# Optimization experiments

Measured on AMD Instinct MI355X. Metric: run time of the kernel, lower is better.

The kernel has to match this reference:

```python
import jax, jax.numpy as jnp
import numpy as np
import math

D = 512
CAT_VOCAB = 512
TIME_START, TIME_STEPS = 512, 1000
NOTE_START, NOTE_RANGE = 1512, 128
VEL_START, VEL_BINS = 1640, 32
DUR_START, DUR_STEPS = 1672, 1000
VOCAB = 2672


def setup_inputs() -> dict:
    key = jax.random.key(0)
    ks = jax.random.split(key, 16)
    tokens = jax.random.randint(ks[0], (8, 8192), 0, VOCAB)
    token_emb = jax.random.normal(ks[1], (CAT_VOCAB, D), jnp.float32) * 0.02
    token_emb = token_emb.at[0].set(0.0)  # padding_idx=0 row is zero
    return {
        'tokens': tokens,
        'token_emb': token_emb,
        'time_lin_w': jax.random.normal(ks[2], (D // 2,), jnp.float32),
        'time_lin_b': jax.random.normal(ks[3], (D // 2,), jnp.float32),
        'time_w': jax.random.normal(ks[4], (D // 2,), jnp.float32),
        'time_b': jax.random.normal(ks[5], (D // 2,), jnp.float32),
        'vel_w1': jax.random.normal(ks[6], (D // 2,), jnp.float32),
        'vel_b1': jax.random.normal(ks[7], (D // 2,), jnp.float32),
        'vel_w2': jax.random.normal(ks[8], (D, D // 2), jnp.float32) * 0.05,
        'vel_b2': jax.random.normal(ks[9], (D,), jnp.float32),
        'vel_ln_g': jnp.ones((D,), jnp.float32),
        'vel_ln_b': jnp.zeros((D,), jnp.float32),
        'dur_lin_w': jax.random.normal(ks[10], (D // 2,), jnp.float32),
        'dur_lin_b': jax.random.normal(ks[11], (D // 2,), jnp.float32),
        'dur_w': jax.random.normal(ks[12], (D // 2,), jnp.float32),
        'dur_b': jax.random.normal(ks[13], (D // 2,), jnp.float32),
    }


def _time2vec(t, max_steps, lin_w, lin_b, w, b):
    tn = t.astype(jnp.float32)[..., None] / max_steps        # [B,S,1]
    linear = tn * lin_w + lin_b                              # [B,S,D/2]
    periodic = jnp.sin(tn * w + b)                           # [B,S,D/2]
    return jnp.concatenate([linear, periodic], axis=-1)


def _pitch_embed(p):
    pf = p.astype(jnp.float32)
    octave = jnp.floor(pf / 12.0)
    semitone = jnp.mod(pf, 12.0)
    i = jnp.arange(D // 4, dtype=jnp.float32)                # [D/4]
    div = 2.0 ** i
    ph_oct = octave[..., None] / div                         # [B,S,D/4]
    ph_sem = semitone[..., None] * (math.pi / 6.0) * (i + 1.0)
    # interleave (sin oct, cos oct, sin sem, cos sem) per group of 4
    emb = jnp.stack([jnp.sin(ph_oct), jnp.cos(ph_oct),
                     jnp.sin(ph_sem), jnp.cos(ph_sem)], axis=-1)
    return emb.reshape(*p.shape, D)


def _vel_embed(v, w1, b1, w2, b2, g, beta):
    vn = v.astype(jnp.float32)[..., None] / VEL_BINS         # [B,S,1]
    h = jax.nn.gelu(vn * w1 + b1, approximate=False)         # [B,S,D/2]
    e = jnp.einsum('bsh,dh->bsd', h, w2) + b2                # [B,S,D]
    mu = e.mean(-1, keepdims=True)
    var = ((e - mu) ** 2).mean(-1, keepdims=True)
    return g * (e - mu) / jnp.sqrt(var + 1e-5) + beta


def reference(tokens, token_emb, time_lin_w, time_lin_b, time_w, time_b,
              vel_w1, vel_b1, vel_w2, vel_b2, vel_ln_g, vel_ln_b,
              dur_lin_w, dur_lin_b, dur_w, dur_b):
    cat_mask = tokens < CAT_VOCAB
    time_mask = (tokens >= TIME_START) & (tokens < TIME_START + TIME_STEPS)
    note_mask = (tokens >= NOTE_START) & (tokens < NOTE_START + NOTE_RANGE)
    vel_mask = (tokens >= VEL_START) & (tokens < VEL_START + VEL_BINS)
    dur_mask = (tokens >= DUR_START) & (tokens < DUR_START + DUR_STEPS)

    safe_idx = jnp.clip(tokens, 0, CAT_VOCAB - 1)
    out = jnp.where(cat_mask[..., None], token_emb[safe_idx], 0.0)

    t_emb = _time2vec(tokens - TIME_START, float(TIME_STEPS),
                      time_lin_w, time_lin_b, time_w, time_b)
    p_emb = _pitch_embed(tokens - NOTE_START)
    v_emb = _vel_embed(tokens - VEL_START, vel_w1, vel_b1, vel_w2, vel_b2,
                       vel_ln_g, vel_ln_b)
    d_emb = _time2vec(tokens - DUR_START, float(DUR_STEPS),
                      dur_lin_w, dur_lin_b, dur_w, dur_b)

    out = jnp.where(time_mask[..., None], t_emb, out)
    out = jnp.where(note_mask[..., None], p_emb, out)
    out = jnp.where(vel_mask[..., None], v_emb, out)
    out = jnp.where(dur_mask[..., None], d_emb, out)
    return out
```

## Files before the change

kernel.cpp:

```cpp
#include <hip/hip_runtime.h>
#include <math.h>

#define DD 512
#define CAT_VOCAB 512
#define TIME_START 512
#define TIME_STEPS 1000
#define NOTE_START 1512
#define NOTE_RANGE 128
#define VEL_START 1640
#define VEL_BINS 32
#define DUR_START 1672
#define DUR_STEPS 1000
#define VOCAB 2672

typedef float f32x4 __attribute__((ext_vector_type(4)));

__device__ __forceinline__ float gelu_exact(float x) {
    return 0.5f * x * (1.0f + erff(x * 0.70710678118654752440f));
}

__device__ __forceinline__ float fsin(float x) {
    float r = x * 0.15915494309189535f;
    r = r - floorf(r);
    return __builtin_amdgcn_sinf(r);
}
__device__ __forceinline__ float fcos(float x) {
    float r = x * 0.15915494309189535f;
    r = r - floorf(r);
    return __builtin_amdgcn_cosf(r);
}

__global__ __launch_bounds__(256) void vel_e_kernel(
    const float* __restrict__ vel_w1, const float* __restrict__ vel_b1,
    const float* __restrict__ vel_w2, const float* __restrict__ vel_b2,
    float* __restrict__ e_tab,
    float* __restrict__ stats)
{
    __shared__ float e_lds[64];

    const int blk = blockIdx.x;
    const int b   = blk >> 3;
    const int o   = blk & 7;
    const float vn = (float)b / 32.0f;
    const int tid = threadIdx.x;
    const int lane = tid & 63;
    const int wave = tid >> 6;

    const float4 w1v = *(const float4*)(vel_w1 + lane * 4);
    const float4 b1v = *(const float4*)(vel_b1 + lane * 4);
    float4 hv;
    hv.x = gelu_exact(vn * w1v.x + b1v.x);
    hv.y = gelu_exact(vn * w1v.y + b1v.y);
    hv.z = gelu_exact(vn * w1v.z + b1v.z);
    hv.w = gelu_exact(vn * w1v.w + b1v.w);

    const int rbase = o * 64 + wave * 16;
    for (int rg = 0; rg < 16; rg += 8) {
        float p[8];
        #pragma unroll
        for (int k = 0; k < 8; ++k) {
            const int d = rbase + rg + k;
            const float4 w2v = *(const float4*)(vel_w2 + (size_t)d * 256 + lane * 4);
            p[k] = w2v.x * hv.x + w2v.y * hv.y + w2v.z * hv.z + w2v.w * hv.w;
        }
        #pragma unroll
        for (int off = 32; off > 0; off >>= 1) {
            #pragma unroll
            for (int k = 0; k < 8; ++k) p[k] += __shfl_xor(p[k], off);
        }
        #pragma unroll
        for (int k = 0; k < 8; ++k) {
            if (lane == k) e_lds[wave * 16 + rg + k] = p[k] + vel_b2[rbase + rg + k];
        }
    }
    __syncthreads();

    if (tid < 64) {
        const float e = e_lds[tid];
        e_tab[(size_t)b * DD + o * 64 + tid] = e;
        float s = e, q = e * e;
        #pragma unroll
        for (int off = 32; off > 0; off >>= 1) {
            s += __shfl_xor(s, off);
            q += __shfl_xor(q, off);
        }
        if (tid == 0) {
            stats[((size_t)b * 8 + o) * 2]     = s;
            stats[((size_t)b * 8 + o) * 2 + 1] = q;
        }
    }
}

__global__ __launch_bounds__(256) void direct_kernel(
    const int* __restrict__ tokens,
    const float* __restrict__ token_emb,
    const float* __restrict__ time_lin_w, const float* __restrict__ time_lin_b,
    const float* __restrict__ time_w,     const float* __restrict__ time_b,
    const float* __restrict__ dur_lin_w,  const float* __restrict__ dur_lin_b,
    const float* __restrict__ dur_w,      const float* __restrict__ dur_b,
    const float* __restrict__ vel_ln_g,   const float* __restrict__ vel_ln_b,
    const float* __restrict__ e_tab,      const float* __restrict__ stats,
    float* __restrict__ out, int total_chunks)
{
    const int c = blockIdx.x * 256 + threadIdx.x;
    if (c >= total_chunks) return;

    const int tok = c >> 7;
    const int ch  = c & 127;
    const int d   = ch * 4;
    const int t   = tokens[tok];

    f32x4 v;

    if (t < CAT_VOCAB) {
        v = *(const f32x4*)(token_emb + (size_t)t * DD + d);
    } else if (t < NOTE_START || t >= DUR_START) {
        const bool is_time = (t < NOTE_START);
        const int start = is_time ? TIME_START : DUR_START;
        const float tn = (float)(t - start) / 1000.0f;
        if (ch < 64) {
            const float* lw = is_time ? time_lin_w : dur_lin_w;
            const float* lb = is_time ? time_lin_b : dur_lin_b;
            const float4 w = *(const float4*)(lw + d);
            const float4 b = *(const float4*)(lb + d);
            v.x = tn * w.x + b.x; v.y = tn * w.y + b.y;
            v.z = tn * w.z + b.z; v.w = tn * w.w + b.w;
        } else {
            const float* pw = is_time ? time_w : dur_w;
            const float* pb = is_time ? time_b : dur_b;
            const float4 w = *(const float4*)(pw + d - 256);
            const float4 b = *(const float4*)(pb + d - 256);
            v.x = fsin(tn * w.x + b.x); v.y = fsin(tn * w.y + b.y);
            v.z = fsin(tn * w.z + b.z); v.w = fsin(tn * w.w + b.w);
        }
    } else if (t < VEL_START) {
        const int p = t - NOTE_START;
        const float oct = (float)(p / 12);
        const float sem = (float)(p % 12);
        const float po = oct * __builtin_amdgcn_exp2f(-(float)ch);
        const float ps = sem * 0.52359877559829887308f * ((float)ch + 1.0f);
        v.x = fsin(po); v.y = fcos(po); v.z = fsin(ps); v.w = fcos(ps);
    } else {
        const int bin = t - VEL_START;
        const f32x4 e = *(const f32x4*)(e_tab + (size_t)bin * DD + d);
        float s = 0.0f, q = 0.0f;
        #pragma unroll
        for (int o = 0; o < 8; ++o) {
            s += stats[((size_t)bin * 8 + o) * 2];
            q += stats[((size_t)bin * 8 + o) * 2 + 1];
        }
        const float mu  = s * (1.0f / 512.0f);
        const float var = q * (1.0f / 512.0f) - mu * mu;
        const float inv = 1.0f / sqrtf(var + 1e-5f);
        const float4 g  = *(const float4*)(vel_ln_g + d);
        const float4 be = *(const float4*)(vel_ln_b + d);
        v.x = g.x * (e.x - mu) * inv + be.x;
        v.y = g.y * (e.y - mu) * inv + be.y;
        v.z = g.z * (e.z - mu) * inv + be.z;
        v.w = g.w * (e.w - mu) * inv + be.w;
    }

    __builtin_nontemporal_store(v, (f32x4*)(out + (size_t)c * 4));
}

__global__ __launch_bounds__(256) void music_emb_fallback(
    const int* __restrict__ tokens,
    const float* __restrict__ token_emb,
    const float* __restrict__ time_lin_w, const float* __restrict__ time_lin_b,
    const float* __restrict__ time_w,     const float* __restrict__ time_b,
    const float* __restrict__ vel_w1,     const float* __restrict__ vel_b1,
    const float* __restrict__ vel_w2,     const float* __restrict__ vel_b2,
    const float* __restrict__ vel_ln_g,   const float* __restrict__ vel_ln_b,
    const float* __restrict__ dur_lin_w,  const float* __restrict__ dur_lin_b,
    const float* __restrict__ dur_w,      const float* __restrict__ dur_b,
    float* __restrict__ out, int n_tokens)
{
    const int wave = threadIdx.x >> 6;
    const int lane = threadIdx.x & 63;
    const int tok_idx = blockIdx.x * 4 + wave;
    if (tok_idx >= n_tokens) return;

    const int t = tokens[tok_idx];
    float* __restrict__ orow = out + (size_t)tok_idx * DD;
    const int d0 = lane * 4;
    const int d1 = 256 + lane * 4;
    float4 r0, r1;

    if (t < CAT_VOCAB) {
        r0 = *(const float4*)(token_emb + (size_t)t * DD + d0);
        r1 = *(const float4*)(token_emb + (size_t)t * DD + d1);
    } else if (t < NOTE_START || (t >= DUR_START && t < DUR_START + DUR_STEPS)) {
        const bool is_time = (t < NOTE_START);
        const float* lw = is_time ? time_lin_w : dur_lin_w;
        const float* lb = is_time ? time_lin_b : dur_lin_b;
        const float* pw = is_time ? time_w    : dur_w;
        const float* pb = is_time ? time_b    : dur_b;
        const int start = is_time ? TIME_START : DUR_START;
        const float tn = (float)(t - start) / 1000.0f;
        float a[4], p[4];
        #pragma unroll
        for (int k = 0; k < 4; ++k) {
            a[k] = tn * lw[d0 + k] + lb[d0 + k];
            p[k] = sinf(tn * pw[d0 + k] + pb[d0 + k]);
        }
        r0 = make_float4(a[0], a[1], a[2], a[3]);
        r1 = make_float4(p[0], p[1], p[2], p[3]);
    } else if (t < NOTE_START + NOTE_RANGE) {
        const int p = t - NOTE_START;
        const float oct = (float)(p / 12);
        const float sem = (float)(p % 12);
        const float cc = 0.52359877559829887308f;
        {
            const float i = (float)lane;
            const float po = oct * exp2f(-i);
            const float ps = (sem * cc) * (i + 1.0f);
            r0 = make_float4(sinf(po), cosf(po), sinf(ps), cosf(ps));
        }
        {
            const float i = (float)(64 + lane);
            const float po = oct * exp2f(-i);
            const float ps = (sem * cc) * (i + 1.0f);
            r1 = make_float4(sinf(po), cosf(po), sinf(ps), cosf(ps));
        }
    } else if (t < VEL_START + VEL_BINS) {
        const float vn = (float)(t - VEL_START) / 32.0f;
        float hj[4];
        #pragma unroll
        for (int k = 0; k < 4; ++k) {
            const float x = vn * vel_w1[d0 + k] + vel_b1[d0 + k];
            hj[k] = gelu_exact(x);
        }
        float e0[4], e1[4];
        #pragma unroll
        for (int k = 0; k < 4; ++k) { e0[k] = vel_b2[d0 + k]; e1[k] = vel_b2[d1 + k]; }
        for (int src = 0; src < 64; ++src) {
            const float h0 = __shfl(hj[0], src);
            const float h1 = __shfl(hj[1], src);
            const float h2 = __shfl(hj[2], src);
            const float h3 = __shfl(hj[3], src);
            const int j = src << 2;
            #pragma unroll
            for (int k = 0; k < 4; ++k) {
                const float4 wa = *(const float4*)(vel_w2 + (size_t)(d0 + k) * 256 + j);
                const float4 wb = *(const float4*)(vel_w2 + (size_t)(d1 + k) * 256 + j);
                e0[k] += h0 * wa.x + h1 * wa.y + h2 * wa.z + h3 * wa.w;
                e1[k] += h0 * wb.x + h1 * wb.y + h2 * wb.z + h3 * wb.w;
            }
        }
        float s1 = 0.0f;
        #pragma unroll
        for (int k = 0; k < 4; ++k) s1 += e0[k] + e1[k];
        #pragma unroll
        for (int off = 32; off > 0; off >>= 1) s1 += __shfl_xor(s1, off);
        const float mu = s1 * (1.0f / 512.0f);
        float s2 = 0.0f;
        #pragma unroll
        for (int k = 0; k < 4; ++k) {
            const float a = e0[k] - mu, bb = e1[k] - mu;
            s2 += a * a + bb * bb;
        }
        #pragma unroll
        for (int off = 32; off > 0; off >>= 1) s2 += __shfl_xor(s2, off);
        const float inv = 1.0f / sqrtf(s2 * (1.0f / 512.0f) + 1e-5f);
        #pragma unroll
        for (int k = 0; k < 4; ++k) {
            e0[k] = vel_ln_g[d0 + k] * (e0[k] - mu) * inv + vel_ln_b[d0 + k];
            e1[k] = vel_ln_g[d1 + k] * (e1[k] - mu) * inv + vel_ln_b[d1 + k];
        }
        r0 = make_float4(e0[0], e0[1], e0[2], e0[3]);
        r1 = make_float4(e1[0], e1[1], e1[2], e1[3]);
    } else {
        r0 = make_float4(0.f, 0.f, 0.f, 0.f);
        r1 = make_float4(0.f, 0.f, 0.f, 0.f);
    }

    *(float4*)(orow + d0) = r0;
    *(float4*)(orow + d1) = r1;
}

extern "C" void kernel_launch(void* const* d_in, const int* in_sizes, int n_in,
                              void* d_out, int out_size, void* d_ws, size_t ws_size,
                              hipStream_t stream) {
    const int*   tokens     = (const int*)  d_in[0];
    const float* token_emb  = (const float*)d_in[1];
    const float* time_lin_w = (const float*)d_in[2];
    const float* time_lin_b = (const float*)d_in[3];
    const float* time_w     = (const float*)d_in[4];
    const float* time_b     = (const float*)d_in[5];
    const float* vel_w1     = (const float*)d_in[6];
    const float* vel_b1     = (const float*)d_in[7];
    const float* vel_w2     = (const float*)d_in[8];
    const float* vel_b2     = (const float*)d_in[9];
    const float* vel_ln_g   = (const float*)d_in[10];
    const float* vel_ln_b   = (const float*)d_in[11];
    const float* dur_lin_w  = (const float*)d_in[12];
    const float* dur_lin_b  = (const float*)d_in[13];
    const float* dur_w      = (const float*)d_in[14];
    const float* dur_b      = (const float*)d_in[15];
    float* out = (float*)d_out;

    const int n_tokens = in_sizes[0];
    const size_t e_bytes     = (size_t)VEL_BINS * DD * sizeof(float);
    const size_t stats_bytes = (size_t)VEL_BINS * 8 * 2 * sizeof(float);

    if (ws_size >= e_bytes + stats_bytes) {
        float* e_tab = (float*)d_ws;
        float* stats = (float*)((char*)d_ws + e_bytes);

        hipLaunchKernelGGL(vel_e_kernel, dim3(VEL_BINS * 8), dim3(256), 0, stream,
                           vel_w1, vel_b1, vel_w2, vel_b2, e_tab, stats);

        const int total_chunks = n_tokens * (DD / 4);
        const int blocks = (total_chunks + 255) / 256;
        hipLaunchKernelGGL(direct_kernel, dim3(blocks), dim3(256), 0, stream,
                           tokens, token_emb,
                           time_lin_w, time_lin_b, time_w, time_b,
                           dur_lin_w, dur_lin_b, dur_w, dur_b,
                           vel_ln_g, vel_ln_b, e_tab, stats,
                           out, total_chunks);
    } else {
        const int blocks = (n_tokens + 3) / 4;
        hipLaunchKernelGGL(music_emb_fallback, dim3(blocks), dim3(256), 0, stream,
                           tokens, token_emb,
                           time_lin_w, time_lin_b, time_w, time_b,
                           vel_w1, vel_b1, vel_w2, vel_b2, vel_ln_g, vel_ln_b,
                           dur_lin_w, dur_lin_b, dur_w, dur_b,
                           out, n_tokens);
    }
}
```

Before: 31.12 us.

## Map one wave per token in direct kernel and split velocity table work finer

The main kernel now gives each token to a single wavefront, with each lane writing two float4 chunks. Before, each thread handled one 4-float chunk. This removes per-chunk branch divergence within a wave, reads the token id once per wave, and merges the linear and periodic halves into one thread. The velocity precompute kernel is split into 16 slices per bin instead of 8, giving twice as many blocks each doing one pass of 8 rows. The fallback kernel switches to fast sin/cos/exp2 intrinsics, and the fast path now requires the token count to be a multiple of 4.

Result: slower. 32.79 us (+5.4%).

```diff
diff --git a/kernel.cpp b/kernel.cpp
--- a/kernel.cpp
+++ b/kernel.cpp
@@ -36,11 +36,11 @@
     float* __restrict__ e_tab,
     float* __restrict__ stats)
 {
-    __shared__ float e_lds[64];
+    __shared__ float e_lds[32];
 
     const int blk = blockIdx.x;
-    const int b   = blk >> 3;
-    const int o   = blk & 7;
+    const int b   = blk >> 4;
+    const int sx  = blk & 15;
     const float vn = (float)b / 32.0f;
     const int tid = threadIdx.x;
     const int lane = tid & 63;
@@ -54,39 +54,36 @@
     hv.z = gelu_exact(vn * w1v.z + b1v.z);
     hv.w = gelu_exact(vn * w1v.w + b1v.w);
 
-    const int rbase = o * 64 + wave * 16;
-    for (int rg = 0; rg < 16; rg += 8) {
-        float p[8];
-        #pragma unroll
-        for (int k = 0; k < 8; ++k) {
-            const int d = rbase + rg + k;
-            const float4 w2v = *(const float4*)(vel_w2 + (size_t)d * 256 + lane * 4);
-            p[k] = w2v.x * hv.x + w2v.y * hv.y + w2v.z * hv.z + w2v.w * hv.w;
-        }
-        #pragma unroll
-        for (int off = 32; off > 0; off >>= 1) {
-            #pragma unroll
-            for (int k = 0; k < 8; ++k) p[k] += __shfl_xor(p[k], off);
-        }
-        #pragma unroll
-        for (int k = 0; k < 8; ++k) {
-            if (lane == k) e_lds[wave * 16 + rg + k] = p[k] + vel_b2[rbase + rg + k];
-        }
+    const int rbase = sx * 32 + wave * 8;
+    float p[8];
+    #pragma unroll
+    for (int k = 0; k < 8; ++k) {
+        const float4 w2v = *(const float4*)(vel_w2 + (size_t)(rbase + k) * 256 + lane * 4);
+        p[k] = w2v.x * hv.x + w2v.y * hv.y + w2v.z * hv.z + w2v.w * hv.w;
+    }
+    #pragma unroll
+    for (int off = 32; off > 0; off >>= 1) {
+        #pragma unroll
+        for (int k = 0; k < 8; ++k) p[k] += __shfl_xor(p[k], off);
+    }
+    #pragma unroll
+    for (int k = 0; k < 8; ++k) {
+        if (lane == k) e_lds[wave * 8 + k] = p[k] + vel_b2[rbase + k];
     }
     __syncthreads();
 
-    if (tid < 64) {
+    if (tid < 32) {
         const float e = e_lds[tid];
-        e_tab[(size_t)b * DD + o * 64 + tid] = e;
+        e_tab[(size_t)b * DD + sx * 32 + tid] = e;
         float s = e, q = e * e;
         #pragma unroll
-        for (int off = 32; off > 0; off >>= 1) {
+        for (int off = 16; off > 0; off >>= 1) {
             s += __shfl_xor(s, off);
             q += __shfl_xor(q, off);
         }
         if (tid == 0) {
-            stats[((size_t)b * 8 + o) * 2]     = s;
-            stats[((size_t)b * 8 + o) * 2 + 1] = q;
+            stats[((size_t)b * 16 + sx) * 2]     = s;
+            stats[((size_t)b * 16 + sx) * 2 + 1] = q;
         }
     }
 }
@@ -100,67 +97,83 @@
     const float* __restrict__ dur_w,      const float* __restrict__ dur_b,
     const float* __restrict__ vel_ln_g,   const float* __restrict__ vel_ln_b,
     const float* __restrict__ e_tab,      const float* __restrict__ stats,
-    float* __restrict__ out, int total_chunks)
+    float* __restrict__ out)
 {
-    const int c = blockIdx.x * 256 + threadIdx.x;
-    if (c >= total_chunks) return;
-
-    const int tok = c >> 7;
-    const int ch  = c & 127;
-    const int d   = ch * 4;
-    const int t   = tokens[tok];
-
-    f32x4 v;
+    const int wave = threadIdx.x >> 6;
+    const int lane = threadIdx.x & 63;
+    const int tok  = blockIdx.x * 4 + wave;
+    const int t    = tokens[tok];
+    float* __restrict__ orow = out + (size_t)tok * DD;
+    const int d0 = lane * 4;
+    const int d1 = 256 + d0;
+
+    f32x4 r0, r1;
 
     if (t < CAT_VOCAB) {
-        v = *(const f32x4*)(token_emb + (size_t)t * DD + d);
+        r0 = *(const f32x4*)(token_emb + (size_t)t * DD + d0);
+        r1 = *(const f32x4*)(token_emb + (size_t)t * DD + d1);
     } else if (t < NOTE_START || t >= DUR_START) {
         const bool is_time = (t < NOTE_START);
         const int start = is_time ? TIME_START : DUR_START;
         const float tn = (float)(t - start) / 1000.0f;
-        if (ch < 64) {
-            const float* lw = is_time ? time_lin_w : dur_lin_w;
-            const float* lb = is_time ? time_lin_b : dur_lin_b;
-            const float4 w = *(const float4*)(lw + d);
-            const float4 b = *(const float4*)(lb + d);
-            v.x = tn * w.x + b.x; v.y = tn * w.y + b.y;
-            v.z = tn * w.z + b.z; v.w = tn * w.w + b.w;
-        } else {
-            const float* pw = is_time ? time_w : dur_w;
-            const float* pb = is_time ? time_b : dur_b;
-            const float4 w = *(const float4*)(pw + d - 256);
-            const float4 b = *(const float4*)(pb + d - 256);
-            v.x = fsin(tn * w.x + b.x); v.y = fsin(tn * w.y + b.y);
-            v.z = fsin(tn * w.z + b.z); v.w = fsin(tn * w.w + b.w);
-        }
+        const float* lw = is_time ? time_lin_w : dur_lin_w;
+        const float* lb = is_time ? time_lin_b : dur_lin_b;
+        const float* pw = is_time ? time_w    : dur_w;
+        const float* pb = is_time ? time_b    : dur_b;
+        const float4 w  = *(const float4*)(lw + d0);
+        const float4 bb = *(const float4*)(lb + d0);
+        const float4 w2 = *(const float4*)(pw + d0);
+        const float4 b2 = *(const float4*)(pb + d0);
+        r0.x = tn * w.x + bb.x;  r0.y = tn * w.y + bb.y;
+        r0.z = tn * w.z + bb.z;  r0.w = tn * w.w + bb.w;
+        r1.x = fsin(tn * w2.x + b2.x); r1.y = fsin(tn * w2.y + b2.y);
+        r1.z = fsin(tn * w2.z + b2.z); r1.w = fsin(tn * w2.w + b2.w);
     } else if (t < VEL_START) {
         const int p = t - NOTE_START;
         const float oct = (float)(p / 12);
         const float sem = (float)(p % 12);
-        const float po = oct * __builtin_amdgcn_exp2f(-(float)ch);
-        const float ps = sem * 0.52359877559829887308f * ((float)ch + 1.0f);
-        v.x = fsin(po); v.y = fcos(po); v.z = fsin(ps); v.w = fcos(ps);
+        const float cc = 0.52359877559829887308f;
+        {
+            const float i = (float)lane;
+            const float po = oct * __builtin_amdgcn_exp2f(-i);
+            const float ps = sem * cc * (i + 1.0f);
+            r0.x = fsin(po); r0.y = fcos(po); r0.z = fsin(ps); r0.w = fcos(ps);
+        }
+        {
+            const float i = (float)(64 + lane);
+            const float po = oct * __builtin_amdgcn_exp2f(-i);
+            const float ps = sem * cc * (i + 1.0f);
+            r1.x = fsin(po); r1.y = fcos(po); r1.z = fsin(ps); r1.w = fcos(ps);
+        }
     } else {
         const int bin = t - VEL_START;
-        const f32x4 e = *(const f32x4*)(e_tab + (size_t)bin * DD + d);
         float s = 0.0f, q = 0.0f;
         #pragma unroll
-        for (int o = 0; o < 8; ++o) {
-            s += stats[((size_t)bin * 8 + o) * 2];
-            q += stats[((size_t)bin * 8 + o) * 2 + 1];
+        for (int o = 0; o < 16; ++o) {
+            s += stats[((size_t)bin * 16 + o) * 2];
+            q += stats[((size_t)bin * 16 + o) * 2 + 1];
         }
         const float mu  = s * (1.0f / 512.0f);
         const float var = q * (1.0f / 512.0f) - mu * mu;
         const float inv = 1.0f / sqrtf(var + 1e-5f);
-        const float4 g  = *(const float4*)(vel_ln_g + d);
-        const float4 be = *(const float4*)(vel_ln_b + d);
-        v.x = g.x * (e.x - mu) * inv + be.x;
-        v.y = g.y * (e.y - mu) * inv + be.y;
-        v.z = g.z * (e.z - mu) * inv + be.z;
-        v.w = g.w * (e.w - mu) * inv + be.w;
-    }
-
-    __builtin_nontemporal_store(v, (f32x4*)(out + (size_t)c * 4));
+        const f32x4 e0 = *(const f32x4*)(e_tab + (size_t)bin * DD + d0);
+        const f32x4 e1 = *(const f32x4*)(e_tab + (size_t)bin * DD + d1);
+        const float4 g0 = *(const float4*)(vel_ln_g + d0);
+        const float4 g1 = *(const float4*)(vel_ln_g + d1);
+        const float4 b0 = *(const float4*)(vel_ln_b + d0);
+        const float4 b1 = *(const float4*)(vel_ln_b + d1);
+        r0.x = g0.x * (e0.x - mu) * inv + b0.x;
+        r0.y = g0.y * (e0.y - mu) * inv + b0.y;
+        r0.z = g0.z * (e0.z - mu) * inv + b0.z;
+        r0.w = g0.w * (e0.w - mu) * inv + b0.w;
+        r1.x = g1.x * (e1.x - mu) * inv + b1.x;
+        r1.y = g1.y * (e1.y - mu) * inv + b1.y;
+        r1.z = g1.z * (e1.z - mu) * inv + b1.z;
+        r1.w = g1.w * (e1.w - mu) * inv + b1.w;
+    }
+
+    __builtin_nontemporal_store(r0, (f32x4*)(orow + d0));
+    __builtin_nontemporal_store(r1, (f32x4*)(orow + d1));
 }
 
 __global__ __launch_bounds__(256) void music_emb_fallback(
@@ -201,7 +214,7 @@
         #pragma unroll
         for (int k = 0; k < 4; ++k) {
             a[k] = tn * lw[d0 + k] + lb[d0 + k];
-            p[k] = sinf(tn * pw[d0 + k] + pb[d0 + k]);
+            p[k] = fsin(tn * pw[d0 + k] + pb[d0 + k]);
         }
         r0 = make_float4(a[0], a[1], a[2], a[3]);
         r1 = make_float4(p[0], p[1], p[2], p[3]);
@@ -212,15 +225,15 @@
         const float cc = 0.52359877559829887308f;
         {
             const float i = (float)lane;
-            const float po = oct * exp2f(-i);
+            const float po = oct * __builtin_amdgcn_exp2f(-i);
             const float ps = (sem * cc) * (i + 1.0f);
-            r0 = make_float4(sinf(po), cosf(po), sinf(ps), cosf(ps));
+            r0 = make_float4(fsin(po), fcos(po), fsin(ps), fcos(ps));
         }
         {
             const float i = (float)(64 + lane);
-            const float po = oct * exp2f(-i);
+            const float po = oct * __builtin_amdgcn_exp2f(-i);
             const float ps = (sem * cc) * (i + 1.0f);
-            r1 = make_float4(sinf(po), cosf(po), sinf(ps), cosf(ps));
+            r1 = make_float4(fsin(po), fcos(po), fsin(ps), fcos(ps));
         }
     } else if (t < VEL_START + VEL_BINS) {
         const float vn = (float)(t - VEL_START) / 32.0f;
@@ -301,23 +314,21 @@
 
     const int n_tokens = in_sizes[0];
     const size_t e_bytes     = (size_t)VEL_BINS * DD * sizeof(float);
-    const size_t stats_bytes = (size_t)VEL_BINS * 8 * 2 * sizeof(float);
-
-    if (ws_size >= e_bytes + stats_bytes) {
+    const size_t stats_bytes = (size_t)VEL_BINS * 16 * 2 * sizeof(float);
+
+    if (ws_size >= e_bytes + stats_bytes && (n_tokens & 3) == 0) {
         float* e_tab = (float*)d_ws;
         float* stats = (float*)((char*)d_ws + e_bytes);
 
-        hipLaunchKernelGGL(vel_e_kernel, dim3(VEL_BINS * 8), dim3(256), 0, stream,
+        hipLaunchKernelGGL(vel_e_kernel, dim3(VEL_BINS * 16), dim3(256), 0, stream,
                            vel_w1, vel_b1, vel_w2, vel_b2, e_tab, stats);
 
-        const int total_chunks = n_tokens * (DD / 4);
-        const int blocks = (total_chunks + 255) / 256;
-        hipLaunchKernelGGL(direct_kernel, dim3(blocks), dim3(256), 0, stream,
+        hipLaunchKernelGGL(direct_kernel, dim3(n_tokens / 4), dim3(256), 0, stream,
                            tokens, token_emb,
                            time_lin_w, time_lin_b, time_w, time_b,
                            dur_lin_w, dur_lin_b, dur_w, dur_b,
                            vel_ln_g, vel_ln_b, e_tab, stats,
-                           out, total_chunks);
+                           out);
     } else {
         const int blocks = (n_tokens + 3) / 4;
         hipLaunchKernelGGL(music_emb_fallback, dim3(blocks), dim3(256), 0, stream,
```
